# Kernel tuning notes

Hardware: AMD Instinct MI355X
Metric: run time of the kernel (lower is better)

## Reference

```python
import jax, jax.numpy as jnp
import numpy as np

IN_FEATURES = 4096
OUT_FEATURES = 4096
LORA_R = 64
LORA_ALPHA = 16
SCALING = LORA_ALPHA / LORA_R  # 0.25


def setup_inputs() -> dict:
    key = jax.random.key(0)
    k_x, k_w, k_s, k_a, k_b = jax.random.split(key, 5)
    x = jax.random.normal(k_x, (4, 2048, IN_FEATURES), dtype=jnp.float32)
    # int8 quantized base weight in [-8, 7] as in the torch buffer init
    weight_quantized = jax.random.randint(k_w, (OUT_FEATURES, IN_FEATURES), -8, 7, dtype=jnp.int8)
    weight_scale = jax.random.normal(k_s, (1,), dtype=jnp.float32)
    lora_A = jax.random.normal(k_a, (LORA_R, IN_FEATURES), dtype=jnp.float32) * 0.01
    # torch init is zeros; use small random values so the LoRA path is exercised
    lora_B = jax.random.normal(k_b, (OUT_FEATURES, LORA_R), dtype=jnp.float32) * 0.01
    return {"x": x, "weight_quantized": weight_quantized, "weight_scale": weight_scale,
            "lora_A": lora_A, "lora_B": lora_B}


def reference(x, weight_quantized, weight_scale, lora_A, lora_B):
    # 1. dequantize base weight on the fly: [out, in]
    w_dequant = weight_quantized.astype(x.dtype) * weight_scale
    # 2. base GEMM: [B, S, in] x [in, out] -> [B, S, out]
    base = jnp.einsum('bsi,oi->bso', x, w_dequant)
    # 3. LoRA low-rank update (dropout is identity in eval mode)
    lora = jnp.einsum('bsr,or->bso', jnp.einsum('bsi,ri->bsr', x, lora_A), lora_B)
    return base + lora * SCALING
```

## Files before the change

### kernel.cpp

```cpp
#include <hip/hip_runtime.h>

#define M_TOT 8192
#define K_TOT 4096
#define N_TOT 4096
#define RANK  64
#define SCALING 0.25f

typedef __bf16 bf16x8 __attribute__((ext_vector_type(8)));
typedef float floatx4 __attribute__((ext_vector_type(4)));
typedef unsigned short ushort8v __attribute__((ext_vector_type(8)));

static __device__ __forceinline__ unsigned short f32_to_bf16(float f) {
  unsigned int u = __float_as_uint(f);
  u += 0x7FFFu + ((u >> 16) & 1u);
  return (unsigned short)(u >> 16);
}

static __device__ __forceinline__ void async_ld16(const void* g, void* l) {
  __builtin_amdgcn_global_load_lds(
      (const __attribute__((address_space(1))) unsigned int*)g,
      (__attribute__((address_space(3))) unsigned int*)l, 16, 0, 0);
}

__global__ __launch_bounds__(256) void cvt_x_kernel(const float4* __restrict__ x,
                                                    ushort8v* __restrict__ xb) {
  int i = blockIdx.x * 256 + threadIdx.x;
  float4 v0 = x[2 * i];
  float4 v1 = x[2 * i + 1];
  ushort8v o;
  o[0] = f32_to_bf16(v0.x); o[1] = f32_to_bf16(v0.y);
  o[2] = f32_to_bf16(v0.z); o[3] = f32_to_bf16(v0.w);
  o[4] = f32_to_bf16(v1.x); o[5] = f32_to_bf16(v1.y);
  o[6] = f32_to_bf16(v1.z); o[7] = f32_to_bf16(v1.w);
  xb[i] = o;
}

__global__ __launch_bounds__(256) void build_weff_kernel(
    const int* __restrict__ wq, const float* __restrict__ scale_p,
    const float* __restrict__ A, const float* __restrict__ B,
    unsigned short* __restrict__ Weff) {
  __shared__ __align__(16) float Bts[64][128];
  __shared__ __align__(16) float As_[64][128];

  const int tid = threadIdx.x;
  const int bo = blockIdx.y * 128;
  const int bk = blockIdx.x * 128;
  const float scale = scale_p[0];

  {
    const int o = tid >> 1;
    const int rh = (tid & 1) * 32;
    const float* gb = B + (size_t)(bo + o) * RANK + rh;
#pragma unroll
    for (int j = 0; j < 8; ++j) {
      float4 v = *(const float4*)(gb + j * 4);
      Bts[rh + j * 4 + 0][o] = v.x;
      Bts[rh + j * 4 + 1][o] = v.y;
      Bts[rh + j * 4 + 2][o] = v.z;
      Bts[rh + j * 4 + 3][o] = v.w;
    }
  }
#pragma unroll
  for (int j = 0; j < 8; ++j) {
    const int ii = j * 1024 + tid * 4;
    const int r = ii >> 7, c = ii & 127;
    *(floatx4*)&As_[r][c] = *(const floatx4*)(A + (size_t)r * K_TOT + bk + c);
  }
  __syncthreads();

  const int to = tid >> 4;
  const int tk = tid & 15;
  float acc[8][8] = {};
#pragma unroll 4
  for (int r = 0; r < RANK; ++r) {
    floatx4 b0 = *(const floatx4*)&Bts[r][to * 8];
    floatx4 b1 = *(const floatx4*)&Bts[r][to * 8 + 4];
    floatx4 a0 = *(const floatx4*)&As_[r][tk * 8];
    floatx4 a1 = *(const floatx4*)&As_[r][tk * 8 + 4];
    float bv[8] = {b0.x, b0.y, b0.z, b0.w, b1.x, b1.y, b1.z, b1.w};
    float av[8] = {a0.x, a0.y, a0.z, a0.w, a1.x, a1.y, a1.z, a1.w};
#pragma unroll
    for (int a = 0; a < 8; ++a)
#pragma unroll
      for (int b = 0; b < 8; ++b) acc[a][b] += bv[a] * av[b];
  }

#pragma unroll
  for (int a = 0; a < 8; ++a) {
    const int o = bo + to * 8 + a;
    const size_t base = (size_t)o * K_TOT + bk + tk * 8;
    const int4 w0 = *(const int4*)(wq + base);
    const int4 w1 = *(const int4*)(wq + base + 4);
    ushort8v st;
    st[0] = f32_to_bf16((float)w0.x * scale + SCALING * acc[a][0]);
    st[1] = f32_to_bf16((float)w0.y * scale + SCALING * acc[a][1]);
    st[2] = f32_to_bf16((float)w0.z * scale + SCALING * acc[a][2]);
    st[3] = f32_to_bf16((float)w0.w * scale + SCALING * acc[a][3]);
    st[4] = f32_to_bf16((float)w1.x * scale + SCALING * acc[a][4]);
    st[5] = f32_to_bf16((float)w1.y * scale + SCALING * acc[a][5]);
    st[6] = f32_to_bf16((float)w1.z * scale + SCALING * acc[a][6]);
    st[7] = f32_to_bf16((float)w1.w * scale + SCALING * acc[a][7]);
    *(ushort8v*)(Weff + base) = st;
  }
}


template <int QM>
static __device__ __forceinline__ void mfma_half(floatx4 (&acc)[8][4],
                                                 const bf16x8 (&af)[4][2],
                                                 const bf16x8 (&bf)[4][2]) {
#pragma unroll
  for (int ks = 0; ks < 2; ++ks)
#pragma unroll
    for (int i = 0; i < 4; ++i)
#pragma unroll
      for (int j = 0; j < 4; ++j)
        acc[QM * 4 + i][j] = __builtin_amdgcn_mfma_f32_16x16x32_bf16(
            af[i][ks], bf[j][ks], acc[QM * 4 + i][j], 0, 0, 0);
}

__global__ __launch_bounds__(512, 2) void gemm_kernel(
    const unsigned short* __restrict__ Xb,
    const unsigned short* __restrict__ Wb,
    float* __restrict__ out) {
  __shared__ __align__(16) unsigned char smem[131072];

  const int tid = threadIdx.x;
  const int lane = tid & 63;
  const int wave = tid >> 6;
  const int wm = wave >> 2;
  const int wn = wave & 3;

  const int bid = blockIdx.x;
  const int swz = (bid & 7) * 64 + (bid >> 3);
  const int bM = (swz >> 4) * 256;
  const int bN = (swz & 15) * 256;

  const int srow = tid >> 3;
  const int scol = ((tid & 7) ^ (srow & 7)) * 8;
  const unsigned short* xs = Xb + (size_t)(bM + srow) * K_TOT + scol;
  const unsigned short* ws = Wb + (size_t)(bN + srow) * K_TOT + scol;

  const int rb = (lane & 15) * 128;
  const int c0 = (((lane >> 4) + 0) ^ (lane & 7)) * 16;
  const int c1 = (((lane >> 4) + 4) ^ (lane & 7)) * 16;
  const int aBase = wm * 16384;
  const int bBase = 32768 + wn * 8192;

  floatx4 acc[8][4] = {};
  bf16x8 af[4][2];
  bf16x8 bf[4][2];

#define BAR() asm volatile("s_barrier" ::: "memory")
#define WAIT_LGKM0() asm volatile("s_waitcnt lgkmcnt(0)" ::: "memory")
#define WAIT_VM(N) asm volatile("s_waitcnt vmcnt(" #N ")" ::: "memory")
#define STAGE_A(BUF, H, S, KO)                                              \
  async_ld16(xs + (size_t)((H) * 128 + (S) * 64) * K_TOT + (KO),            \
             smem + (BUF) * 65536 + (H) * 16384 + (S) * 8192 + tid * 16)
#define STAGE_B(BUF, H, S, KO)                                              \
  async_ld16(ws + (size_t)((H) * 128 + (S) * 64) * K_TOT + (KO),            \
             smem + (BUF) * 65536 + 32768 + (H) * 16384 + (S) * 8192 + tid * 16)
#define DSR_A(BUF, QM, II, KS)                                              \
  af[II][KS] = *(const bf16x8*)(smem + (BUF) * 65536 + aBase +              \
                                ((QM) * 4 + (II)) * 2048 + rb + ((KS) ? c1 : c0))
#define DSR_B(BUF, J, KS)                                                   \
  bf[J][KS] = *(const bf16x8*)(smem + (BUF) * 65536 + bBase +               \
                               (J) * 2048 + rb + ((KS) ? c1 : c0))

#define ALPHA(BUF, KA)                                                      \
  {                                                                         \
    STAGE_A((BUF) ^ 1, 0, 0, KA); STAGE_A((BUF) ^ 1, 0, 1, KA);             \
    STAGE_A((BUF) ^ 1, 1, 0, KA); STAGE_A((BUF) ^ 1, 1, 1, KA);             \
    DSR_B(BUF, 0, 0); DSR_B(BUF, 1, 0);                                     \
    DSR_A(BUF, 0, 0, 0); DSR_A(BUF, 0, 1, 0);                               \
    DSR_B(BUF, 2, 0); DSR_B(BUF, 3, 0);                                     \
    DSR_A(BUF, 0, 2, 0); DSR_A(BUF, 0, 3, 0);                               \
    DSR_B(BUF, 0, 1); DSR_B(BUF, 1, 1);                                     \
    DSR_A(BUF, 0, 0, 1); DSR_A(BUF, 0, 1, 1);                               \
    DSR_B(BUF, 2, 1); DSR_B(BUF, 3, 1);                                     \
    DSR_A(BUF, 0, 2, 1); DSR_A(BUF, 0, 3, 1);                               \
    __builtin_amdgcn_s_setprio(1);                                          \
    mfma_half<0>(acc, af, bf);                                              \
    __builtin_amdgcn_s_setprio(0);                                          \
    WAIT_LGKM0(); BAR();                                                    \
  }

#define BETA(BUF, KB)                                                       \
  {                                                                         \
    STAGE_B(BUF, 0, 0, KB); STAGE_B(BUF, 0, 1, KB);                         \
    STAGE_B(BUF, 1, 0, KB); STAGE_B(BUF, 1, 1, KB);                         \
    DSR_A(BUF, 1, 0, 0); DSR_A(BUF, 1, 1, 0);                               \
    DSR_A(BUF, 1, 2, 0); DSR_A(BUF, 1, 3, 0);                               \
    DSR_A(BUF, 1, 0, 1); DSR_A(BUF, 1, 1, 1);                               \
    DSR_A(BUF, 1, 2, 1); DSR_A(BUF, 1, 3, 1);                               \
    __builtin_amdgcn_s_setprio(1);                                          \
    mfma_half<1>(acc, af, bf);                                              \
    __builtin_amdgcn_s_setprio(0);                                          \
    WAIT_LGKM0(); WAIT_VM(4); BAR();                                        \
  }

  STAGE_A(0, 0, 0, 0); STAGE_A(0, 0, 1, 0);
  STAGE_A(0, 1, 0, 0); STAGE_A(0, 1, 1, 0);
  STAGE_B(0, 0, 0, 0); STAGE_B(0, 0, 1, 0);
  STAGE_B(0, 1, 0, 0); STAGE_B(0, 1, 1, 0);
  STAGE_B(1, 0, 0, 64); STAGE_B(1, 0, 1, 64);
  STAGE_B(1, 1, 0, 64); STAGE_B(1, 1, 1, 64);
  WAIT_VM(0);
  BAR();

  for (int kt = 0; kt < 64; kt += 2) {
    const int ka0 = ((kt + 1) & 63) * 64;
    const int kb0 = ((kt + 2) & 63) * 64;
    const int ka1 = ((kt + 2) & 63) * 64;
    const int kb1 = ((kt + 3) & 63) * 64;
    ALPHA(0, ka0); BETA(0, kb0);
    ALPHA(1, ka1); BETA(1, kb1);
  }
  WAIT_VM(0);

  const int row0 = bM + wm * 128 + ((lane >> 4) << 2);
  const int col0 = bN + wn * 64 + (lane & 15);
#pragma unroll
  for (int i = 0; i < 8; ++i) {
#pragma unroll
    for (int j = 0; j < 4; ++j) {
#pragma unroll
      for (int r = 0; r < 4; ++r) {
        out[(size_t)(row0 + i * 16 + r) * N_TOT + (col0 + j * 16)] = acc[i][j][r];
      }
    }
  }
#undef BAR
#undef WAIT_LGKM0
#undef WAIT_VM
#undef STAGE_A
#undef STAGE_B
#undef DSR_A
#undef DSR_B
#undef ALPHA
#undef BETA
}

extern "C" void kernel_launch(void* const* d_in, const int* in_sizes, int n_in,
                              void* d_out, int out_size, void* d_ws, size_t ws_size,
                              hipStream_t stream) {
  const float* x      = (const float*)d_in[0];
  const int*   wq     = (const int*)d_in[1];
  const float* wscale = (const float*)d_in[2];
  const float* lora_A = (const float*)d_in[3];
  const float* lora_B = (const float*)d_in[4];
  float* out = (float*)d_out;

  unsigned short* xb   = (unsigned short*)d_ws;
  unsigned short* weff = (unsigned short*)((char*)d_ws + (size_t)M_TOT * K_TOT * 2);

  cvt_x_kernel<<<16384, 256, 0, stream>>>((const float4*)x, (ushort8v*)xb);
  build_weff_kernel<<<dim3(K_TOT / 128, N_TOT / 128), 256, 0, stream>>>(
      wq, wscale, lora_A, lora_B, weff);
  gemm_kernel<<<512, 512, 0, stream>>>(xb, weff, out);
}
```

Before: 496.1 us.

## Split GEMM main loop into four-phase pipeline with finer-grained staging

Restructures the main loop from two phases per K-tile into four, each covering one M-half and one k-substep. A-fragment registers drop from 4x2 to 4, and global-to-LDS async loads are spread across the phases at a different cadence. The aim is to lower register pressure and interleave LDS reads, async staging and MFMA work more finely. The cost is more barriers per tile and a tighter buffer-reuse ordering that must stay correct.

```diff
diff --git a/kernel.cpp b/kernel.cpp
--- a/kernel.cpp
+++ b/kernel.cpp
@@ -105,18 +105,16 @@
 }
 
 
-template <int QM>
-static __device__ __forceinline__ void mfma_half(floatx4 (&acc)[8][4],
-                                                 const bf16x8 (&af)[4][2],
-                                                 const bf16x8 (&bf)[4][2]) {
-#pragma unroll
-  for (int ks = 0; ks < 2; ++ks)
-#pragma unroll
-    for (int i = 0; i < 4; ++i)
-#pragma unroll
-      for (int j = 0; j < 4; ++j)
-        acc[QM * 4 + i][j] = __builtin_amdgcn_mfma_f32_16x16x32_bf16(
-            af[i][ks], bf[j][ks], acc[QM * 4 + i][j], 0, 0, 0);
+template <int QM, int KS>
+static __device__ __forceinline__ void mfma_q(floatx4 (&acc)[8][4],
+                                              const bf16x8 (&af)[4],
+                                              const bf16x8 (&bf)[4][2]) {
+#pragma unroll
+  for (int i = 0; i < 4; ++i)
+#pragma unroll
+    for (int j = 0; j < 4; ++j)
+      acc[QM * 4 + i][j] = __builtin_amdgcn_mfma_f32_16x16x32_bf16(
+          af[i], bf[j][KS], acc[QM * 4 + i][j], 0, 0, 0);
 }
 
 __global__ __launch_bounds__(512, 2) void gemm_kernel(
@@ -148,12 +146,14 @@
   const int bBase = 32768 + wn * 8192;
 
   floatx4 acc[8][4] = {};
-  bf16x8 af[4][2];
+  bf16x8 af[4];
   bf16x8 bf[4][2];
 
 #define BAR() asm volatile("s_barrier" ::: "memory")
 #define WAIT_LGKM0() asm volatile("s_waitcnt lgkmcnt(0)" ::: "memory")
 #define WAIT_VM(N) asm volatile("s_waitcnt vmcnt(" #N ")" ::: "memory")
+#define SP1() __builtin_amdgcn_s_setprio(1)
+#define SP0() __builtin_amdgcn_s_setprio(0)
 #define STAGE_A(BUF, H, S, KO)                                              \
   async_ld16(xs + (size_t)((H) * 128 + (S) * 64) * K_TOT + (KO),            \
              smem + (BUF) * 65536 + (H) * 16384 + (S) * 8192 + tid * 16)
@@ -161,60 +161,55 @@
   async_ld16(ws + (size_t)((H) * 128 + (S) * 64) * K_TOT + (KO),            \
              smem + (BUF) * 65536 + 32768 + (H) * 16384 + (S) * 8192 + tid * 16)
 #define DSR_A(BUF, QM, II, KS)                                              \
-  af[II][KS] = *(const bf16x8*)(smem + (BUF) * 65536 + aBase +              \
-                                ((QM) * 4 + (II)) * 2048 + rb + ((KS) ? c1 : c0))
+  af[II] = *(const bf16x8*)(smem + (BUF) * 65536 + aBase +                  \
+                            ((QM) * 4 + (II)) * 2048 + rb + ((KS) ? c1 : c0))
 #define DSR_B(BUF, J, KS)                                                   \
   bf[J][KS] = *(const bf16x8*)(smem + (BUF) * 65536 + bBase +               \
                                (J) * 2048 + rb + ((KS) ? c1 : c0))
-
-#define ALPHA(BUF, KA)                                                      \
-  {                                                                         \
-    STAGE_A((BUF) ^ 1, 0, 0, KA); STAGE_A((BUF) ^ 1, 0, 1, KA);             \
-    STAGE_A((BUF) ^ 1, 1, 0, KA); STAGE_A((BUF) ^ 1, 1, 1, KA);             \
-    DSR_B(BUF, 0, 0); DSR_B(BUF, 1, 0);                                     \
-    DSR_A(BUF, 0, 0, 0); DSR_A(BUF, 0, 1, 0);                               \
-    DSR_B(BUF, 2, 0); DSR_B(BUF, 3, 0);                                     \
-    DSR_A(BUF, 0, 2, 0); DSR_A(BUF, 0, 3, 0);                               \
-    DSR_B(BUF, 0, 1); DSR_B(BUF, 1, 1);                                     \
-    DSR_A(BUF, 0, 0, 1); DSR_A(BUF, 0, 1, 1);                               \
-    DSR_B(BUF, 2, 1); DSR_B(BUF, 3, 1);                                     \
-    DSR_A(BUF, 0, 2, 1); DSR_A(BUF, 0, 3, 1);                               \
-    __builtin_amdgcn_s_setprio(1);                                          \
-    mfma_half<0>(acc, af, bf);                                              \
-    __builtin_amdgcn_s_setprio(0);                                          \
-    WAIT_LGKM0(); BAR();                                                    \
-  }
-
-#define BETA(BUF, KB)                                                       \
-  {                                                                         \
-    STAGE_B(BUF, 0, 0, KB); STAGE_B(BUF, 0, 1, KB);                         \
-    STAGE_B(BUF, 1, 0, KB); STAGE_B(BUF, 1, 1, KB);                         \
-    DSR_A(BUF, 1, 0, 0); DSR_A(BUF, 1, 1, 0);                               \
-    DSR_A(BUF, 1, 2, 0); DSR_A(BUF, 1, 3, 0);                               \
-    DSR_A(BUF, 1, 0, 1); DSR_A(BUF, 1, 1, 1);                               \
-    DSR_A(BUF, 1, 2, 1); DSR_A(BUF, 1, 3, 1);                               \
-    __builtin_amdgcn_s_setprio(1);                                          \
-    mfma_half<1>(acc, af, bf);                                              \
-    __builtin_amdgcn_s_setprio(0);                                          \
-    WAIT_LGKM0(); WAIT_VM(4); BAR();                                        \
-  }
+#define DSR_A4(BUF, QM, KS)                                                 \
+  DSR_A(BUF, QM, 0, KS); DSR_A(BUF, QM, 1, KS);                             \
+  DSR_A(BUF, QM, 2, KS); DSR_A(BUF, QM, 3, KS)
+#define DSR_B4(BUF, KS)                                                     \
+  DSR_B(BUF, 0, KS); DSR_B(BUF, 1, KS); DSR_B(BUF, 2, KS); DSR_B(BUF, 3, KS)
+#define CORE(QM, KS)                                                        \
+  BAR(); WAIT_LGKM0(); SP1(); mfma_q<QM, KS>(acc, af, bf); SP0()
 
   STAGE_A(0, 0, 0, 0); STAGE_A(0, 0, 1, 0);
   STAGE_A(0, 1, 0, 0); STAGE_A(0, 1, 1, 0);
   STAGE_B(0, 0, 0, 0); STAGE_B(0, 0, 1, 0);
   STAGE_B(0, 1, 0, 0); STAGE_B(0, 1, 1, 0);
   STAGE_B(1, 0, 0, 64); STAGE_B(1, 0, 1, 64);
-  STAGE_B(1, 1, 0, 64); STAGE_B(1, 1, 1, 64);
   WAIT_VM(0);
   BAR();
 
   for (int kt = 0; kt < 64; kt += 2) {
-    const int ka0 = ((kt + 1) & 63) * 64;
-    const int kb0 = ((kt + 2) & 63) * 64;
-    const int ka1 = ((kt + 2) & 63) * 64;
-    const int kb1 = ((kt + 3) & 63) * 64;
-    ALPHA(0, ka0); BETA(0, kb0);
-    ALPHA(1, ka1); BETA(1, kb1);
+    const int k1 = ((kt + 1) & 63) * 64;
+    const int k2 = ((kt + 2) & 63) * 64;
+    const int k3 = ((kt + 3) & 63) * 64;
+    DSR_B4(0, 0); DSR_A4(0, 0, 0);
+    STAGE_B(1, 1, 0, k1); STAGE_B(1, 1, 1, k1);
+    STAGE_A(1, 0, 0, k1); STAGE_A(1, 0, 1, k1);
+    CORE(0, 0); BAR();
+    DSR_A4(0, 1, 0);
+    STAGE_A(1, 1, 0, k1); STAGE_A(1, 1, 1, k1);
+    CORE(1, 0); BAR();
+    DSR_B4(0, 1); DSR_A4(0, 0, 1);
+    CORE(0, 1); BAR();
+    DSR_A4(0, 1, 1);
+    STAGE_B(0, 0, 0, k2); STAGE_B(0, 0, 1, k2);
+    CORE(1, 1); WAIT_VM(2); BAR();
+    DSR_B4(1, 0); DSR_A4(1, 0, 0);
+    STAGE_B(0, 1, 0, k2); STAGE_B(0, 1, 1, k2);
+    STAGE_A(0, 0, 0, k2); STAGE_A(0, 0, 1, k2);
+    CORE(0, 0); BAR();
+    DSR_A4(1, 1, 0);
+    STAGE_A(0, 1, 0, k2); STAGE_A(0, 1, 1, k2);
+    CORE(1, 0); BAR();
+    DSR_B4(1, 1); DSR_A4(1, 0, 1);
+    CORE(0, 1); BAR();
+    DSR_A4(1, 1, 1);
+    STAGE_B(1, 0, 0, k3); STAGE_B(1, 0, 1, k3);
+    CORE(1, 1); WAIT_VM(2); BAR();
   }
   WAIT_VM(0);
 
@@ -233,12 +228,15 @@
 #undef BAR
 #undef WAIT_LGKM0
 #undef WAIT_VM
+#undef SP1
+#undef SP0
 #undef STAGE_A
 #undef STAGE_B
 #undef DSR_A
 #undef DSR_B
-#undef ALPHA
-#undef BETA
+#undef DSR_A4
+#undef DSR_B4
+#undef CORE
 }
 
 extern "C" void kernel_launch(void* const* d_in, const int* in_sizes, int n_in,
```

New measurement: 503.3 us. About the same (+1.4%).
